# Performance work log

Measured on AMD Instinct MI355X. Metric: run time of the kernel, lower is better.

The kernel has to match this reference:

```python
import jax, jax.numpy as jnp
import numpy as np
import math

D = 256        # input_size == d_k == d_v (per the module: d_k = input_size)
H = 4          # n_heads
MAX_LEN = 800  # PositionalEncoding max_len
NEG = float(-(2**32) + 1)
LN_EPS = 1e-5


def _make_pe():
    pe = np.zeros((MAX_LEN, D), dtype=np.float32)
    pos = np.arange(MAX_LEN, dtype=np.float32)[:, None]
    div = np.exp(np.arange(0, D, 2, dtype=np.float32) * -(math.log(10000.0) / D))
    pe[:, 0::2] = np.sin(pos * div)
    pe[:, 1::2] = np.cos(pos * div)
    return jnp.asarray(pe)


def setup_inputs() -> dict:
    key = jax.random.key(0)
    ks = jax.random.split(key, 12)
    B, L = 32, 512

    def xavier(k, shape):
        fan_in, fan_out = shape[0], shape[1]
        std = math.sqrt(2.0 / (fan_in + fan_out))
        return jax.random.normal(k, shape, dtype=jnp.float32) * std

    return {
        "Q": jax.random.normal(ks[0], (B, L, D), dtype=jnp.float32),
        "K": jax.random.normal(ks[1], (B, L, D), dtype=jnp.float32),
        "V": jax.random.normal(ks[2], (B, L, D), dtype=jnp.float32),
        "mask": jax.random.randint(ks[3], (B, L), 0, 2).astype(jnp.bool_),
        "pe": _make_pe(),
        "W_q": xavier(ks[4], (D, H * D)),
        "W_k": xavier(ks[5], (D, H * D)),
        "W_v": xavier(ks[6], (D, H * D)),
        "W_o": xavier(ks[7], (H * D, D)),
        "w1": xavier(ks[8], (D, D)),
        "b1": jnp.zeros((D,), dtype=jnp.float32),
        "w2": xavier(ks[9], (D, D)),
        "b2": jnp.zeros((D,), dtype=jnp.float32),
        "gamma": jnp.ones((D,), dtype=jnp.float32),
        "beta": jnp.zeros((D,), dtype=jnp.float32),
    }


def _layer_norm(x, gamma, beta):
    mu = jnp.mean(x, axis=-1, keepdims=True)
    var = jnp.mean(jnp.square(x - mu), axis=-1, keepdims=True)
    return (x - mu) * jax.lax.rsqrt(var + LN_EPS) * gamma + beta


def _mha(Q, K, V, mask, W_q, W_k, W_v, W_o):
    B, Lq, _ = Q.shape
    Lk = K.shape[1]

    def split_heads(X, W, L):
        # (B, L, D) @ (D, H*D) -> (B*H, L, D)
        return (X @ W).reshape(B, L, H, D).transpose(0, 2, 1, 3).reshape(B * H, L, D)

    Qh = split_heads(Q, W_q, Lq)
    Kh = split_heads(K, W_k, Lk)
    Vh = split_heads(V, W_v, Lk)

    scale = D ** 0.5 + 1e-6
    scores = jnp.einsum('bqd,bkd->bqk', Qh, Kh) / scale  # (B*H, Lq, Lk)

    pad = jnp.broadcast_to(mask[:, None, :], (B, H, Lq)).reshape(B * H, Lq)
    pad_mask = jnp.broadcast_to(pad[:, :, None], (B * H, Lq, Lk))
    causal = jnp.triu(jnp.ones((Lq, Lk), dtype=jnp.bool_), k=1)
    full_mask = causal[None] | pad_mask
    scores = jnp.where(full_mask, NEG, scores)

    att = jax.nn.softmax(scores, axis=-1)
    Vatt = jnp.einsum('bqk,bkd->bqd', att, Vh)  # (B*H, Lq, D)
    Vatt = Vatt.reshape(B, H, Lq, D).transpose(0, 2, 1, 3).reshape(B, Lq, H * D)
    return Vatt @ W_o


def reference(Q, K, V, mask, pe, W_q, W_k, W_v, W_o, w1, b1, w2, b2, gamma, beta):
    Lq, Lk, Lv = Q.shape[1], K.shape[1], V.shape[1]
    Qp = Q + pe[None, :Lq]
    Kp = K + pe[None, :Lk]
    Vp = V + pe[None, :Lv]

    Vatt = _mha(Qp, Kp, Vp, mask, W_q, W_k, W_v, W_o)
    X = _layer_norm(Qp + Vatt, gamma, beta)
    ffn = jax.nn.relu(X @ w1.T + b1) @ w2.T + b2
    return _layer_norm(ffn + X, gamma, beta)
```

## Files before the change

### kernel.cpp

```cpp
#include <hip/hip_runtime.h>
#include <stdint.h>

#define SEQ   512
#define DM    256
#define NB    32
#define NH    4
#define HD    (NH * DM)
#define PE_MASK (SEQ * DM - 1)
#define NEGV  (-4294967295.0f)

typedef __attribute__((ext_vector_type(8))) short short8;
typedef __attribute__((ext_vector_type(4))) float f32x4;

#if defined(__has_builtin)
#if __has_builtin(__builtin_amdgcn_global_load_lds)
#define HAS_ASYNC 1
#endif
#endif
#ifndef HAS_ASYNC
#define HAS_ASYNC 0
#endif

__device__ __forceinline__ float b2f(unsigned short u) {
    return __uint_as_float(((uint32_t)u) << 16);
}
__device__ __forceinline__ unsigned short f2b(float f) {
    uint32_t u = __float_as_uint(f);
    u += 0x7fffu + ((u >> 16) & 1u);
    return (unsigned short)(u >> 16);
}

__global__ __launch_bounds__(256) void mask_canon(
    const unsigned char* __restrict__ raw, int* __restrict__ canon)
{
    __shared__ int enc_byte, enc_odd;
    int tid = threadIdx.x;
    if (tid == 0) { enc_byte = 0; enc_odd = 0; }
    __syncthreads();
    if (tid < 255 && raw[tid * 4 + 1]) atomicOr(&enc_byte, 1);
    if (tid < 128 && ((const int*)raw)[tid * 2 + 1]) atomicOr(&enc_odd, 1);
    __syncthreads();
    int i = blockIdx.x * 256 + tid;
    int v;
    if (enc_byte)      v = (raw[i] != 0);
    else if (enc_odd)  v = (((const int*)raw)[i] != 0);
    else               v = ((((const int*)raw)[i * 2] | ((const int*)raw)[i * 2 + 1]) != 0);
    canon[i] = v;
}

__global__ __launch_bounds__(256) void addpe_f2b(
    const float* __restrict__ X, const float* __restrict__ pe,
    unsigned short* __restrict__ out)
{
    long i = (long)(blockIdx.x * 256 + threadIdx.x) * 4;
    float4 x = *reinterpret_cast<const float4*>(X + i);
    float4 p = *reinterpret_cast<const float4*>(pe + (i & PE_MASK));
    ushort4 o;
    o.x = f2b(x.x + p.x); o.y = f2b(x.y + p.y);
    o.z = f2b(x.z + p.z); o.w = f2b(x.w + p.w);
    *reinterpret_cast<ushort4*>(out + i) = o;
}

__global__ __launch_bounds__(256) void conv_f2b(
    const float* __restrict__ in, unsigned short* __restrict__ out)
{
    long i = (long)(blockIdx.x * 256 + threadIdx.x) * 4;
    float4 x = *reinterpret_cast<const float4*>(in + i);
    ushort4 o;
    o.x = f2b(x.x); o.y = f2b(x.y); o.z = f2b(x.z); o.w = f2b(x.w);
    *reinterpret_cast<ushort4*>(out + i) = o;
}

__global__ __launch_bounds__(256) void transpose_f2b(
    const float* __restrict__ in, unsigned short* __restrict__ out,
    int ldin, int ldout)
{
    __shared__ unsigned short tile[32][33];
    int r0 = blockIdx.y * 32, c0 = blockIdx.x * 32;
    int i = threadIdx.x >> 3;
    int j = (threadIdx.x & 7) * 4;
    float4 v = *reinterpret_cast<const float4*>(in + (long)(r0 + i) * ldin + c0 + j);
    tile[i][j + 0] = f2b(v.x); tile[i][j + 1] = f2b(v.y);
    tile[i][j + 2] = f2b(v.z); tile[i][j + 3] = f2b(v.w);
    __syncthreads();
    ushort4 w;
    w.x = tile[j + 0][i]; w.y = tile[j + 1][i]; w.z = tile[j + 2][i]; w.w = tile[j + 3][i];
    *reinterpret_cast<ushort4*>(out + (long)(c0 + i) * ldout + r0 + j) = w;
}

__global__ __launch_bounds__(256) void transpose_bf16(
    const unsigned short* __restrict__ in, unsigned short* __restrict__ out,
    int ldin, int ldout, long sInB, long sInH, long sOutB, long sOutH, int Hdiv)
{
    int z = blockIdx.z; int b = z / Hdiv; int h = z % Hdiv;
    const unsigned short* ip = in + b * sInB + h * sInH;
    unsigned short* op = out + b * sOutB + h * sOutH;
    __shared__ unsigned short tile[32][33];
    int r0 = blockIdx.y * 32, c0 = blockIdx.x * 32;
    int i = threadIdx.x >> 3;
    int j = (threadIdx.x & 7) * 4;
    ushort4 v = *reinterpret_cast<const ushort4*>(ip + (long)(r0 + i) * ldin + c0 + j);
    tile[i][j + 0] = v.x; tile[i][j + 1] = v.y; tile[i][j + 2] = v.z; tile[i][j + 3] = v.w;
    __syncthreads();
    ushort4 w;
    w.x = tile[j + 0][i]; w.y = tile[j + 1][i]; w.z = tile[j + 2][i]; w.w = tile[j + 3][i];
    *reinterpret_cast<ushort4*>(op + (long)(c0 + i) * ldout + r0 + j) = w;
}

template<bool BIAS, bool RELU, bool OUTBF16>
__global__ __launch_bounds__(256) void gemm_bt(
    const unsigned short* __restrict__ A, int lda,
    const unsigned short* __restrict__ B, int ldb,
    void* __restrict__ Cv, int ldc,
    const float* __restrict__ bias, float scale, int K, int Hdiv,
    long sAb, long sAh, long sAz,
    long sBb, long sBh, long sBz,
    long sCb, long sCh, long sCz)
{
    const int m0 = blockIdx.y * 128;
    const int n0 = blockIdx.x * 128;
    int z  = blockIdx.z;
    int bb = z / Hdiv, hh = z % Hdiv;
    const unsigned short* Ab = A + bb * sAb + hh * sAh + (long)z * sAz;
    const unsigned short* Bb = B + bb * sBb + hh * sBh + (long)z * sBz;
    long coff = bb * sCb + hh * sCh + (long)z * sCz;

    __shared__ unsigned short As[128 * 32];
    __shared__ unsigned short Bs[128 * 32];

    const int tid  = threadIdx.x;
    const int lane = tid & 63;
    const int wave = tid >> 6;
    const int wm   = (wave >> 1) * 64;
    const int wn   = (wave & 1) * 64;
    const int lm   = lane & 15;
    const int kq   = (lane >> 4) * 8;

    f32x4 acc[4][4] = {};

    for (int k0 = 0; k0 < K; k0 += 32) {
#pragma unroll
        for (int it = 0; it < 2; ++it) {
            int id = tid + it * 256;
            int r  = id >> 2;
            int c8 = (id & 3) * 8;
            const unsigned short* gA = Ab + (long)(m0 + r) * lda + k0 + c8;
            const unsigned short* gB = Bb + (long)(n0 + r) * ldb + k0 + c8;
#if HAS_ASYNC
            unsigned short* lA = &As[(size_t)(it * 256 + wave * 64) * 8];
            unsigned short* lB = &Bs[(size_t)(it * 256 + wave * 64) * 8];
            __builtin_amdgcn_global_load_lds(
                (const __attribute__((address_space(1))) void*)gA,
                (__attribute__((address_space(3))) void*)lA, 16, 0, 0);
            __builtin_amdgcn_global_load_lds(
                (const __attribute__((address_space(1))) void*)gB,
                (__attribute__((address_space(3))) void*)lB, 16, 0, 0);
#else
            *reinterpret_cast<uint4*>(&As[(size_t)id * 8]) =
                *reinterpret_cast<const uint4*>(gA);
            *reinterpret_cast<uint4*>(&Bs[(size_t)id * 8]) =
                *reinterpret_cast<const uint4*>(gB);
#endif
        }
        __syncthreads();

        short8 af[4], bfr[4];
#pragma unroll
        for (int i = 0; i < 4; ++i)
            af[i] = *reinterpret_cast<const short8*>(&As[(wm + i * 16 + lm) * 32 + kq]);
#pragma unroll
        for (int j = 0; j < 4; ++j)
            bfr[j] = *reinterpret_cast<const short8*>(&Bs[(wn + j * 16 + lm) * 32 + kq]);
#pragma unroll
        for (int i = 0; i < 4; ++i)
#pragma unroll
            for (int j = 0; j < 4; ++j)
                acc[i][j] = __builtin_amdgcn_mfma_f32_16x16x32_bf16(af[i], bfr[j], acc[i][j], 0, 0, 0);
        __syncthreads();
    }

#pragma unroll
    for (int j = 0; j < 4; ++j) {
        int col  = n0 + wn + j * 16 + lm;
        float bv = 0.f;
        if (BIAS) bv = bias[col];
#pragma unroll
        for (int i = 0; i < 4; ++i) {
#pragma unroll
            for (int r = 0; r < 4; ++r) {
                int row = m0 + wm + i * 16 + (lane >> 4) * 4 + r;
                float v = acc[i][j][r] * scale + bv;
                if (RELU) v = fmaxf(v, 0.f);
                long idx = coff + (long)row * ldc + col;
                if (OUTBF16) reinterpret_cast<unsigned short*>(Cv)[idx] = f2b(v);
                else         reinterpret_cast<float*>(Cv)[idx] = v;
            }
        }
    }
}

__global__ __launch_bounds__(256) void flash_attn(
    const unsigned short* __restrict__ Qh,
    const unsigned short* __restrict__ Kh,
    const unsigned short* __restrict__ VhT,
    unsigned short* __restrict__ Vatt,
    const int* __restrict__ maskc, int bh0, float scale, int nbh)
{
    const int tid  = threadIdx.x;
    const int lane = tid & 63;
    const int wave = tid >> 6;
    const int lm   = lane & 15;
    const int qg   = lane >> 4;
    const int kq   = qg * 8;

    const int L   = blockIdx.x;
    const int z   = L % nbh;
    const int qt  = L / nbh;
    const int b_l = z >> 2, h = z & 3;
    const int m0  = qt * 64;
    const int wq0 = m0 + wave * 16;
    const long qkbase = (long)b_l * SEQ * HD + (long)h * DM;
    const unsigned short* Aq = Qh + qkbase;
    const unsigned short* Ak = Kh + qkbase;
    const unsigned short* Av = VhT + (long)b_l * SEQ * HD + (long)h * SEQ * DM;
    unsigned short* Ov = Vatt + qkbase;
    const int bglob = (bh0 + z) >> 2;

    __shared__ unsigned short Ks[SEQ * 32];
    __shared__ __align__(16) unsigned short Pw[4][16][40];

    f32x4 S[32] = {};
    const int NT = (m0 >> 4) + wave + 1;

    for (int kc = 0; kc < 8; ++kc) {
        for (int it = 0; it <= qt; ++it) {
            int id = tid + it * 256;
            const unsigned short* g = Ak + (long)(id >> 2) * HD + kc * 32 + (id & 3) * 8;
#if HAS_ASYNC
            unsigned short* l = &Ks[(size_t)(it * 256 + wave * 64) * 8];
            __builtin_amdgcn_global_load_lds(
                (const __attribute__((address_space(1))) void*)g,
                (__attribute__((address_space(3))) void*)l, 16, 0, 0);
#else
            *reinterpret_cast<uint4*>(&Ks[(size_t)id * 8]) =
                *reinterpret_cast<const uint4*>(g);
#endif
        }
        short8 qf = *reinterpret_cast<const short8*>(
            Aq + (long)(wq0 + lm) * HD + kc * 32 + kq);
        __syncthreads();
#pragma unroll
        for (int nt = 0; nt < 32; ++nt) {
            if (nt < NT) {
                short8 bf = *reinterpret_cast<const short8*>(&Ks[(nt * 16 + lm) * 32 + kq]);
                S[nt] = __builtin_amdgcn_mfma_f32_16x16x32_bf16(qf, bf, S[nt], 0, 0, 0);
            }
        }
        __syncthreads();
    }

    int   qrow[4];
    bool  rowm[4];
    float mx[4], sm[4];
#pragma unroll
    for (int r = 0; r < 4; ++r) {
        int q = wq0 + qg * 4 + r;
        qrow[r] = q;
        rowm[r] = maskc[bglob * SEQ + q] != 0;
        mx[r] = -3.4e38f;
    }
#pragma unroll
    for (int nt = 0; nt < 32; ++nt) {
        int k = nt * 16 + lm;
#pragma unroll
        for (int r = 0; r < 4; ++r) {
            float v = S[nt][r] * scale;
            if (k > qrow[r] || rowm[r]) v = NEGV;
            S[nt][r] = v;
            mx[r] = fmaxf(mx[r], v);
        }
    }
#pragma unroll
    for (int r = 0; r < 4; ++r) {
#pragma unroll
        for (int off = 8; off >= 1; off >>= 1)
            mx[r] = fmaxf(mx[r], __shfl_xor(mx[r], off));
        sm[r] = 0.f;
    }
#pragma unroll
    for (int nt = 0; nt < 32; ++nt)
#pragma unroll
        for (int r = 0; r < 4; ++r) {
            float e = __expf(S[nt][r] - mx[r]);
            S[nt][r] = e;
            sm[r] += e;
        }
#pragma unroll
    for (int r = 0; r < 4; ++r) {
#pragma unroll
        for (int off = 8; off >= 1; off >>= 1)
            sm[r] += __shfl_xor(sm[r], off);
        sm[r] = 1.0f / sm[r];
    }
#pragma unroll
    for (int nt = 0; nt < 32; ++nt)
#pragma unroll
        for (int r = 0; r < 4; ++r) S[nt][r] *= sm[r];

    f32x4 O[16] = {};
    unsigned short* Vs = Ks;
    for (int kc2 = 0; kc2 < 16; ++kc2) {
#pragma unroll
        for (int it = 0; it < 4; ++it) {
            int id = tid + it * 256;
            const unsigned short* g = Av + (long)(id >> 2) * SEQ + kc2 * 32 + (id & 3) * 8;
#if HAS_ASYNC
            unsigned short* l = &Vs[(size_t)(it * 256 + wave * 64) * 8];
            __builtin_amdgcn_global_load_lds(
                (const __attribute__((address_space(1))) void*)g,
                (__attribute__((address_space(3))) void*)l, 16, 0, 0);
#else
            *reinterpret_cast<uint4*>(&Vs[(size_t)id * 8]) =
                *reinterpret_cast<const uint4*>(g);
#endif
        }
#pragma unroll
        for (int t = 0; t < 2; ++t) {
            int nt = kc2 * 2 + t;
#pragma unroll
            for (int r = 0; r < 4; ++r)
                Pw[wave][qg * 4 + r][t * 16 + lm] = f2b(S[nt][r]);
        }
        __syncthreads();
        short8 pf = *reinterpret_cast<const short8*>(&Pw[wave][lm][kq]);
#pragma unroll
        for (int nt2 = 0; nt2 < 16; ++nt2) {
            short8 vf = *reinterpret_cast<const short8*>(&Vs[(nt2 * 16 + lm) * 32 + kq]);
            O[nt2] = __builtin_amdgcn_mfma_f32_16x16x32_bf16(pf, vf, O[nt2], 0, 0, 0);
        }
        __syncthreads();
    }

#pragma unroll
    for (int nt2 = 0; nt2 < 16; ++nt2) {
#pragma unroll
        for (int r = 0; r < 4; ++r) {
            int l = wq0 + qg * 4 + r;
            Ov[(long)l * HD + nt2 * 16 + lm] = f2b(O[nt2][r]);
        }
    }
}

__global__ __launch_bounds__(256) void ln1_kernel(
    const unsigned short* __restrict__ AttO, const float* __restrict__ Q,
    const float* __restrict__ pe,
    const float* __restrict__ gamma, const float* __restrict__ beta,
    float* __restrict__ outf, unsigned short* __restrict__ outb)
{
    int row  = blockIdx.x * 4 + (threadIdx.x >> 6);
    int lane = threadIdx.x & 63;
    long base = (long)row * DM + lane * 4;
    ushort4 a = *reinterpret_cast<const ushort4*>(AttO + base);
    float4 qv = *reinterpret_cast<const float4*>(Q + base);
    float4 pv = *reinterpret_cast<const float4*>(pe + (base & PE_MASK));
    float x[4] = {b2f(a.x) + qv.x + pv.x, b2f(a.y) + qv.y + pv.y,
                  b2f(a.z) + qv.z + pv.z, b2f(a.w) + qv.w + pv.w};
    float s = x[0] + x[1] + x[2] + x[3];
#pragma unroll
    for (int off = 32; off > 0; off >>= 1) s += __shfl_xor(s, off);
    float mu = s * (1.0f / DM);
    float vs = 0.f;
#pragma unroll
    for (int t = 0; t < 4; ++t) { float d = x[t] - mu; vs += d * d; }
#pragma unroll
    for (int off = 32; off > 0; off >>= 1) vs += __shfl_xor(vs, off);
    float inv = rsqrtf(vs * (1.0f / DM) + 1e-5f);
    int d0 = lane * 4;
    float4 g = *reinterpret_cast<const float4*>(gamma + d0);
    float4 bt = *reinterpret_cast<const float4*>(beta + d0);
    float4 o;
    o.x = (x[0] - mu) * inv * g.x + bt.x;
    o.y = (x[1] - mu) * inv * g.y + bt.y;
    o.z = (x[2] - mu) * inv * g.z + bt.z;
    o.w = (x[3] - mu) * inv * g.w + bt.w;
    *reinterpret_cast<float4*>(outf + base) = o;
    ushort4 ob;
    ob.x = f2b(o.x); ob.y = f2b(o.y); ob.z = f2b(o.z); ob.w = f2b(o.w);
    *reinterpret_cast<ushort4*>(outb + base) = ob;
}

__global__ __launch_bounds__(256) void ln2_kernel(
    const float* __restrict__ F, const float* __restrict__ X,
    const float* __restrict__ gamma, const float* __restrict__ beta,
    float* __restrict__ out)
{
    int row  = blockIdx.x * 4 + (threadIdx.x >> 6);
    int lane = threadIdx.x & 63;
    long base = (long)row * DM + lane * 4;
    float4 a = *reinterpret_cast<const float4*>(F + base);
    float4 c = *reinterpret_cast<const float4*>(X + base);
    float x[4] = {a.x + c.x, a.y + c.y, a.z + c.z, a.w + c.w};
    float s = x[0] + x[1] + x[2] + x[3];
#pragma unroll
    for (int off = 32; off > 0; off >>= 1) s += __shfl_xor(s, off);
    float mu = s * (1.0f / DM);
    float vs = 0.f;
#pragma unroll
    for (int t = 0; t < 4; ++t) { float d = x[t] - mu; vs += d * d; }
#pragma unroll
    for (int off = 32; off > 0; off >>= 1) vs += __shfl_xor(vs, off);
    float inv = rsqrtf(vs * (1.0f / DM) + 1e-5f);
    int d0 = lane * 4;
    float4 g = *reinterpret_cast<const float4*>(gamma + d0);
    float4 bt = *reinterpret_cast<const float4*>(beta + d0);
    float4 o;
    o.x = (x[0] - mu) * inv * g.x + bt.x;
    o.y = (x[1] - mu) * inv * g.y + bt.y;
    o.z = (x[2] - mu) * inv * g.z + bt.z;
    o.w = (x[3] - mu) * inv * g.w + bt.w;
    *reinterpret_cast<float4*>(out + base) = o;
}

extern "C" void kernel_launch(void* const* d_in, const int* in_sizes, int n_in,
                              void* d_out, int out_size, void* d_ws, size_t ws_size,
                              hipStream_t stream)
{
    const float* Q  = (const float*)d_in[0];
    const float* Ki = (const float*)d_in[1];
    const float* Vi = (const float*)d_in[2];
    const unsigned char* mask_raw = (const unsigned char*)d_in[3];
    const float* pe = (const float*)d_in[4];
    const float* Wq = (const float*)d_in[5];
    const float* Wk = (const float*)d_in[6];
    const float* Wv = (const float*)d_in[7];
    const float* Wo = (const float*)d_in[8];
    const float* w1 = (const float*)d_in[9];
    const float* b1 = (const float*)d_in[10];
    const float* w2 = (const float*)d_in[11];
    const float* b2 = (const float*)d_in[12];
    const float* gamma = (const float*)d_in[13];
    const float* beta  = (const float*)d_in[14];
    float* out = (float*)d_out;

    const size_t MiB = 1048576;
    char* ws = (char*)d_ws;

    int CB = 1;
    for (int cb = 32; cb >= 1; cb >>= 1) {
        size_t scr_sz = (size_t)(5 * cb) * MiB;
        if (scr_sz < 24 * MiB) scr_sz = 24 * MiB;
        if ((59 * MiB + scr_sz) <= ws_size) { CB = cb; break; }
    }
    const int NCH = NB / CB;

    unsigned short* WqT  = (unsigned short*)(ws);
    unsigned short* WkT  = WqT + 262144;
    unsigned short* WvT  = WkT + 262144;
    unsigned short* WoT  = WvT + 262144;
    unsigned short* w1b  = (unsigned short*)(ws + 2 * MiB);
    unsigned short* w2b  = w1b + 65536;
    int*            maskc = (int*)(ws + 2 * MiB + 262144);
    unsigned short* Qp   = (unsigned short*)(ws + 3 * MiB);
    unsigned short* Kp   = (unsigned short*)(ws + 11 * MiB);
    unsigned short* Vp   = (unsigned short*)(ws + 19 * MiB);
    unsigned short* AttO = (unsigned short*)(ws + 27 * MiB);
    unsigned short* Xb   = (unsigned short*)(ws + 35 * MiB);
    float*          Xf   = (float*)(ws + 43 * MiB);
    char*           scr  = ws + 59 * MiB;
    unsigned short* Qh   = (unsigned short*)(scr);
    unsigned short* Kh   = (unsigned short*)(scr + (size_t)CB * MiB);
    unsigned short* Vh   = (unsigned short*)(scr + (size_t)2 * CB * MiB);
    unsigned short* VhT  = (unsigned short*)(scr + (size_t)3 * CB * MiB);
    unsigned short* Vatt = (unsigned short*)(scr + (size_t)4 * CB * MiB);
    unsigned short* H1   = (unsigned short*)(scr);
    float*          Ff   = (float*)(scr + 8 * MiB);

    const float scale = (float)(1.0 / (16.0 + 1e-6));
    const long CROWS = (long)CB * SEQ;
    const long CBELT = (long)CB * MiB / 2;

    mask_canon<<<64, 256, 0, stream>>>(mask_raw, maskc);
    transpose_f2b<<<dim3(32, 8, 1), 256, 0, stream>>>(Wq, WqT, HD, DM);
    transpose_f2b<<<dim3(32, 8, 1), 256, 0, stream>>>(Wk, WkT, HD, DM);
    transpose_f2b<<<dim3(32, 8, 1), 256, 0, stream>>>(Wv, WvT, HD, DM);
    transpose_f2b<<<dim3(8, 32, 1), 256, 0, stream>>>(Wo, WoT, DM, HD);
    conv_f2b<<<64, 256, 0, stream>>>(w1, w1b);
    conv_f2b<<<64, 256, 0, stream>>>(w2, w2b);
    addpe_f2b<<<4096, 256, 0, stream>>>(Q,  pe, Qp);
    addpe_f2b<<<4096, 256, 0, stream>>>(Ki, pe, Kp);
    addpe_f2b<<<4096, 256, 0, stream>>>(Vi, pe, Vp);

    for (int c = 0; c < NCH; ++c) {
        const long r0   = (long)c * CROWS;
        const int  bh0  = c * CB * NH;
        const int  gy   = (int)(CROWS / 128);
        const int  nbh  = CB * NH;

        gemm_bt<false, false, true><<<dim3(8, gy, 3), 256, 0, stream>>>(
            Qp + r0 * DM, DM, WqT, DM, Qh, HD, nullptr, 1.f, DM,
            1, 4194304, 0, 0, 262144, 0, 0, CBELT, 0, 0);

        transpose_bf16<<<dim3(8, 16, CB * NH), 256, 0, stream>>>(
            Vh, VhT, HD, SEQ, (long)SEQ * HD, DM, (long)SEQ * HD, (long)SEQ * DM, NH);

        flash_attn<<<dim3(8 * nbh, 1, 1), 256, 0, stream>>>(
            Qh, Kh, VhT, Vatt, maskc, bh0, scale, nbh);

        gemm_bt<false, false, true><<<dim3(2, gy, 1), 256, 0, stream>>>(
            Vatt, HD, WoT, HD, AttO + r0 * DM, DM, nullptr, 1.f, HD,
            1, 0,0,0, 0,0,0, 0,0,0);
    }

    ln1_kernel<<<4096, 256, 0, stream>>>(AttO, Q, pe, gamma, beta, Xf, Xb);

    gemm_bt<true, true, true><<<dim3(2, 128, 1), 256, 0, stream>>>(
        Xb, DM, w1b, DM, H1, DM, b1, 1.f, DM, 1, 0,0,0, 0,0,0, 0,0,0);
    gemm_bt<true, false, false><<<dim3(2, 128, 1), 256, 0, stream>>>(
        H1, DM, w2b, DM, Ff, DM, b2, 1.f, DM, 1, 0,0,0, 0,0,0, 0,0,0);

    ln2_kernel<<<4096, 256, 0, stream>>>(Ff, Xf, gamma, beta, out);
}
```

Baseline: 388.7 us.

## Double-buffer V tiles in flash attention, remap block order, batch prep kernels

```diff
diff --git a/kernel.cpp b/kernel.cpp
--- a/kernel.cpp
+++ b/kernel.cpp
@@ -48,27 +48,58 @@
     canon[i] = v;
 }
 
-__global__ __launch_bounds__(256) void addpe_f2b(
-    const float* __restrict__ X, const float* __restrict__ pe,
-    unsigned short* __restrict__ out)
-{
-    long i = (long)(blockIdx.x * 256 + threadIdx.x) * 4;
+__global__ __launch_bounds__(256) void addpe3(
+    const float* __restrict__ Q, const float* __restrict__ K,
+    const float* __restrict__ V, const float* __restrict__ pe,
+    unsigned short* __restrict__ Qp, unsigned short* __restrict__ Kp,
+    unsigned short* __restrict__ Vp)
+{
+    int blk = blockIdx.x;
+    int seg = blk >> 12;
+    const float* X = (seg == 0) ? Q : (seg == 1) ? K : V;
+    unsigned short* O = (seg == 0) ? Qp : (seg == 1) ? Kp : Vp;
+    long i = (long)((blk & 4095) * 256 + threadIdx.x) * 4;
     float4 x = *reinterpret_cast<const float4*>(X + i);
     float4 p = *reinterpret_cast<const float4*>(pe + (i & PE_MASK));
     ushort4 o;
     o.x = f2b(x.x + p.x); o.y = f2b(x.y + p.y);
     o.z = f2b(x.z + p.z); o.w = f2b(x.w + p.w);
-    *reinterpret_cast<ushort4*>(out + i) = o;
-}
-
-__global__ __launch_bounds__(256) void conv_f2b(
-    const float* __restrict__ in, unsigned short* __restrict__ out)
-{
-    long i = (long)(blockIdx.x * 256 + threadIdx.x) * 4;
+    *reinterpret_cast<ushort4*>(O + i) = o;
+}
+
+__global__ __launch_bounds__(256) void conv2(
+    const float* __restrict__ w1, const float* __restrict__ w2,
+    unsigned short* __restrict__ o1, unsigned short* __restrict__ o2)
+{
+    int blk = blockIdx.x;
+    const float* in = (blk < 64) ? w1 : w2;
+    unsigned short* out = (blk < 64) ? o1 : o2;
+    long i = (long)((blk & 63) * 256 + threadIdx.x) * 4;
     float4 x = *reinterpret_cast<const float4*>(in + i);
     ushort4 o;
     o.x = f2b(x.x); o.y = f2b(x.y); o.z = f2b(x.z); o.w = f2b(x.w);
     *reinterpret_cast<ushort4*>(out + i) = o;
+}
+
+__global__ __launch_bounds__(256) void transpose_f2b3(
+    const float* __restrict__ in0, const float* __restrict__ in1,
+    const float* __restrict__ in2, unsigned short* __restrict__ out,
+    int ldin, int ldout, long outStride)
+{
+    int z = blockIdx.z;
+    const float* in = (z == 0) ? in0 : (z == 1) ? in1 : in2;
+    unsigned short* op = out + z * outStride;
+    __shared__ unsigned short tile[32][33];
+    int r0 = blockIdx.y * 32, c0 = blockIdx.x * 32;
+    int i = threadIdx.x >> 3;
+    int j = (threadIdx.x & 7) * 4;
+    float4 v = *reinterpret_cast<const float4*>(in + (long)(r0 + i) * ldin + c0 + j);
+    tile[i][j + 0] = f2b(v.x); tile[i][j + 1] = f2b(v.y);
+    tile[i][j + 2] = f2b(v.z); tile[i][j + 3] = f2b(v.w);
+    __syncthreads();
+    ushort4 w;
+    w.x = tile[j + 0][i]; w.y = tile[j + 1][i]; w.z = tile[j + 2][i]; w.w = tile[j + 3][i];
+    *reinterpret_cast<ushort4*>(op + (long)(c0 + i) * ldout + r0 + j) = w;
 }
 
 __global__ __launch_bounds__(256) void transpose_f2b(
@@ -213,9 +244,15 @@
     const int qg   = lane >> 4;
     const int kq   = qg * 8;
 
-    const int L   = blockIdx.x;
-    const int z   = L % nbh;
-    const int qt  = L / nbh;
+    const int L = blockIdx.x;
+    int z, qt;
+    if ((nbh & 7) == 0) {
+        int x = L & 7, m = L >> 3;
+        qt = m & 7;
+        z  = x + 8 * (m >> 3);
+    } else {
+        z = L % nbh; qt = L / nbh;
+    }
     const int b_l = z >> 2, h = z & 3;
     const int m0  = qt * 64;
     const int wq0 = m0 + wave * 16;
@@ -259,6 +296,23 @@
         __syncthreads();
     }
 
+    unsigned short* Vb0 = Ks;
+    unsigned short* Vb1 = Ks + 8192;
+#pragma unroll
+    for (int it = 0; it < 4; ++it) {
+        int id = tid + it * 256;
+        const unsigned short* g = Av + (long)(id >> 2) * SEQ + (id & 3) * 8;
+#if HAS_ASYNC
+        unsigned short* l = &Vb0[(size_t)(it * 256 + wave * 64) * 8];
+        __builtin_amdgcn_global_load_lds(
+            (const __attribute__((address_space(1))) void*)g,
+            (__attribute__((address_space(3))) void*)l, 16, 0, 0);
+#else
+        *reinterpret_cast<uint4*>(&Vb0[(size_t)id * 8]) =
+            *reinterpret_cast<const uint4*>(g);
+#endif
+    }
+
     int   qrow[4];
     bool  rowm[4];
     float mx[4], sm[4];
@@ -308,21 +362,26 @@
         for (int r = 0; r < 4; ++r) S[nt][r] *= sm[r];
 
     f32x4 O[16] = {};
-    unsigned short* Vs = Ks;
     for (int kc2 = 0; kc2 < 16; ++kc2) {
-#pragma unroll
-        for (int it = 0; it < 4; ++it) {
-            int id = tid + it * 256;
-            const unsigned short* g = Av + (long)(id >> 2) * SEQ + kc2 * 32 + (id & 3) * 8;
+        unsigned short* Vcur = (kc2 & 1) ? Vb1 : Vb0;
+        __syncthreads();
+        if (kc2 < 15) {
+            unsigned short* Vnext = (kc2 & 1) ? Vb0 : Vb1;
+#pragma unroll
+            for (int it = 0; it < 4; ++it) {
+                int id = tid + it * 256;
+                const unsigned short* g =
+                    Av + (long)(id >> 2) * SEQ + (kc2 + 1) * 32 + (id & 3) * 8;
 #if HAS_ASYNC
-            unsigned short* l = &Vs[(size_t)(it * 256 + wave * 64) * 8];
-            __builtin_amdgcn_global_load_lds(
-                (const __attribute__((address_space(1))) void*)g,
-                (__attribute__((address_space(3))) void*)l, 16, 0, 0);
+                unsigned short* l = &Vnext[(size_t)(it * 256 + wave * 64) * 8];
+                __builtin_amdgcn_global_load_lds(
+                    (const __attribute__((address_space(1))) void*)g,
+                    (__attribute__((address_space(3))) void*)l, 16, 0, 0);
 #else
-            *reinterpret_cast<uint4*>(&Vs[(size_t)id * 8]) =
-                *reinterpret_cast<const uint4*>(g);
-#endif
+                *reinterpret_cast<uint4*>(&Vnext[(size_t)id * 8]) =
+                    *reinterpret_cast<const uint4*>(g);
+#endif
+            }
         }
 #pragma unroll
         for (int t = 0; t < 2; ++t) {
@@ -331,14 +390,12 @@
             for (int r = 0; r < 4; ++r)
                 Pw[wave][qg * 4 + r][t * 16 + lm] = f2b(S[nt][r]);
         }
-        __syncthreads();
         short8 pf = *reinterpret_cast<const short8*>(&Pw[wave][lm][kq]);
 #pragma unroll
         for (int nt2 = 0; nt2 < 16; ++nt2) {
-            short8 vf = *reinterpret_cast<const short8*>(&Vs[(nt2 * 16 + lm) * 32 + kq]);
+            short8 vf = *reinterpret_cast<const short8*>(&Vcur[(nt2 * 16 + lm) * 32 + kq]);
             O[nt2] = __builtin_amdgcn_mfma_f32_16x16x32_bf16(pf, vf, O[nt2], 0, 0, 0);
         }
-        __syncthreads();
     }
 
 #pragma unroll
@@ -480,15 +537,10 @@
     const long CBELT = (long)CB * MiB / 2;
 
     mask_canon<<<64, 256, 0, stream>>>(mask_raw, maskc);
-    transpose_f2b<<<dim3(32, 8, 1), 256, 0, stream>>>(Wq, WqT, HD, DM);
-    transpose_f2b<<<dim3(32, 8, 1), 256, 0, stream>>>(Wk, WkT, HD, DM);
-    transpose_f2b<<<dim3(32, 8, 1), 256, 0, stream>>>(Wv, WvT, HD, DM);
+    transpose_f2b3<<<dim3(32, 8, 3), 256, 0, stream>>>(Wq, Wk, Wv, WqT, HD, DM, 262144);
     transpose_f2b<<<dim3(8, 32, 1), 256, 0, stream>>>(Wo, WoT, DM, HD);
-    conv_f2b<<<64, 256, 0, stream>>>(w1, w1b);
-    conv_f2b<<<64, 256, 0, stream>>>(w2, w2b);
-    addpe_f2b<<<4096, 256, 0, stream>>>(Q,  pe, Qp);
-    addpe_f2b<<<4096, 256, 0, stream>>>(Ki, pe, Kp);
-    addpe_f2b<<<4096, 256, 0, stream>>>(Vi, pe, Vp);
+    conv2<<<128, 256, 0, stream>>>(w1, w2, w1b, w2b);
+    addpe3<<<12288, 256, 0, stream>>>(Q, Ki, Vi, pe, Qp, Kp, Vp);
 
     for (int c = 0; c < NCH; ++c) {
         const long r0   = (long)c * CROWS;
```

Measured after the change: 387.1 us. About the same (-0.4%).
